# Kernel optimization log

Hardware: AMD Instinct MI355X
Metric: run time of the kernel (lower is better)

The kernel has to match this reference:

```python
import jax, jax.numpy as jnp
import numpy as np
import math

HIDDEN = 1024
HEADS = 16

def setup_inputs() -> dict:
    key = jax.random.key(0)
    k1, k2, k3 = jax.random.split(key, 3)
    B, T, C = 4, 2048, HIDDEN
    x = jax.random.normal(k1, (B, T, C), dtype=jnp.float32)
    w_qkv = jax.random.normal(k2, (C, 3 * C), dtype=jnp.float32) * (1.0 / math.sqrt(C))
    b_qkv = jnp.zeros((3 * C,), dtype=jnp.float32)
    w_out = jax.random.normal(k3, (C, C), dtype=jnp.float32) * (1.0 / math.sqrt(C))
    b_out = jnp.zeros((C,), dtype=jnp.float32)
    return {"x": x, "w_qkv": w_qkv, "b_qkv": b_qkv, "w_out": w_out, "b_out": b_out}

def reference(x, w_qkv, b_qkv, w_out, b_out):
    B, T, C = x.shape
    H = HEADS
    D = C // H  # head dim
    qkv = x @ w_qkv + b_qkv  # [B,T,3C]
    q, k, v = jnp.split(qkv, 3, axis=2)
    # [B,T,C] -> [B,H,T,D]
    q = q.reshape(B, T, H, D).transpose(0, 2, 1, 3)
    k = k.reshape(B, T, H, D).transpose(0, 2, 1, 3)
    v = v.reshape(B, T, H, D).transpose(0, 2, 1, 3)
    scale = 1.0 / math.sqrt(D)
    logits = jnp.einsum('bhqd,bhkd->bhqk', q, k) * scale  # [B,H,T,T]
    causal = jnp.tril(jnp.ones((T, T), dtype=bool))
    logits = jnp.where(causal[None, None, :, :], logits, -jnp.inf)
    probs = jax.nn.softmax(logits, axis=-1)
    out = jnp.einsum('bhqk,bhkd->bhqd', probs, v)  # [B,H,T,D]
    out = out.transpose(0, 2, 1, 3).reshape(B, T, C)
    return out @ w_out + b_out
```

## Files before the change

### kernel.cpp

```cpp
#include <hip/hip_runtime.h>
#include <hip/hip_bf16.h>

#define C_DIM  1024
#define NHEAD  16
#define DHEAD  64
#define T_LEN  2048
#define B_SZ   4
#define M_ROWS (B_SZ * T_LEN)
#define QKV_N  (3 * C_DIM)

typedef __bf16 bf16x8 __attribute__((ext_vector_type(8)));
typedef float  f32x4  __attribute__((ext_vector_type(4)));
typedef unsigned short ushort8_t __attribute__((ext_vector_type(8)));
typedef unsigned int   uint4_t   __attribute__((ext_vector_type(4)));

__device__ __forceinline__ unsigned short f2bf(float f) {
    union { float f; unsigned int u; } v; v.f = f;
    unsigned int r = v.u + 0x7FFFu + ((v.u >> 16) & 1u);
    return (unsigned short)(r >> 16);
}

__device__ __forceinline__ bf16x8 as_bf16x8(ushort8_t u) {
    return __builtin_bit_cast(bf16x8, u);
}

__device__ __forceinline__ f32x4 mfma16(bf16x8 a, bf16x8 b, f32x4 c) {
    return __builtin_amdgcn_mfma_f32_16x16x32_bf16(a, b, c, 0, 0, 0);
}

__device__ __forceinline__ void block_sync_lds() {
    asm volatile("s_waitcnt lgkmcnt(0)" ::: "memory");
    __builtin_amdgcn_s_barrier();
}

#define GLL16(gsrc, ldst) __builtin_amdgcn_global_load_lds( \
    (const __attribute__((address_space(1))) void*)(gsrc),  \
    (__attribute__((address_space(3))) void*)(ldst), 16, 0, 0)

__device__ __forceinline__ int xcd_remap(int id, int nwg) {
    const int q = nwg >> 3, r = nwg & 7;
    const int xcd = id & 7, off = id >> 3;
    return (xcd < r) ? (xcd * (q + 1) + off) : (r * (q + 1) + (xcd - r) * q + off);
}

__global__ void k_convert(const float* __restrict__ in, unsigned short* __restrict__ out, int n4) {
    int i = blockIdx.x * blockDim.x + threadIdx.x;
    if (i >= n4) return;
    const float4 v = ((const float4*)in)[i];
    unsigned int lo = (unsigned int)f2bf(v.x) | ((unsigned int)f2bf(v.y) << 16);
    unsigned int hi = (unsigned int)f2bf(v.z) | ((unsigned int)f2bf(v.w) << 16);
    ((uint2*)out)[i] = make_uint2(lo, hi);
}

__global__ void k_transpose_bf16(const float* __restrict__ w, unsigned short* __restrict__ wT,
                                 int K, int N) {
    __shared__ float tile[32][33];
    const int n0 = blockIdx.x * 32, k0 = blockIdx.y * 32;
    const int tx = threadIdx.x, ty = threadIdx.y;
    for (int i = 0; i < 32; i += 8)
        tile[ty + i][tx] = w[(size_t)(k0 + ty + i) * N + (n0 + tx)];
    __syncthreads();
    for (int i = 0; i < 32; i += 8)
        wT[(size_t)(n0 + ty + i) * K + (k0 + tx)] = f2bf(tile[tx][ty + i]);
}

__global__ void k_transpose_v(const unsigned short* __restrict__ qkv,
                              unsigned short* __restrict__ vtg) {
    __shared__ unsigned short tile[32][33];
    const int tt = blockIdx.x;
    const int dy = blockIdx.y;
    const int bh = dy >> 1, dtile = dy & 1;
    const int b = bh >> 4, h = bh & 15;
    const int t0 = tt * 32, d0 = dtile * 32;
    const int tx = threadIdx.x, ty = threadIdx.y;
    const unsigned short* src = qkv + (size_t)b * T_LEN * QKV_N + 2 * C_DIM + h * DHEAD + d0;
    for (int i = 0; i < 32; i += 8)
        tile[ty + i][tx] = src[(size_t)(t0 + ty + i) * QKV_N + tx];
    __syncthreads();
    unsigned short* dst = vtg + ((size_t)bh * DHEAD + d0) * T_LEN + t0;
    for (int i = 0; i < 32; i += 8)
        dst[(size_t)(ty + i) * T_LEN + tx] = tile[tx][ty + i];
}

template<int BF16_OUT>
__global__ __launch_bounds__(256) void k_gemm(const unsigned short* __restrict__ A,
                       const unsigned short* __restrict__ Bt,
                       const float* __restrict__ bias,
                       void* __restrict__ C,
                       unsigned short* __restrict__ vtg,
                       int M, int N, int K) {
    __shared__ unsigned short As[128][64];
    __shared__ unsigned short Bs[128][64];

    const int tid  = threadIdx.x;
    const int lane = tid & 63;
    const int wv   = tid >> 6;
    const int wm = wv >> 1, wn = wv & 1;

    const int nwg = gridDim.x * gridDim.y;
    const int wg  = xcd_remap(blockIdx.y * gridDim.x + blockIdx.x, nwg);
    const int bx = wg % gridDim.x, by = wg / gridDim.x;
    const int m0 = by * 128;
    const int n0 = bx * 128;
    const int lr = lane & 15, lg = lane >> 4;

    f32x4 acc[4][4];
#pragma unroll
    for (int i = 0; i < 4; i++)
#pragma unroll
        for (int j = 0; j < 4; j++) acc[i][j] = (f32x4){0.f, 0.f, 0.f, 0.f};

    const int gr = lane >> 3;
    const int gc = 8 * ((lane & 7) ^ gr);

    for (int kt = 0; kt < K; kt += 64) {
        __syncthreads();
#pragma unroll
        for (int j = 0; j < 4; j++) {
            const int row = 32 * wv + 8 * j;
            GLL16(A  + (size_t)(m0 + row + gr) * K + kt + gc, &As[row][0]);
            GLL16(Bt + (size_t)(n0 + row + gr) * K + kt + gc, &Bs[row][0]);
        }
        __syncthreads();

#pragma unroll
        for (int s = 0; s < 2; s++) {
            const int cb = (s * 64 + lg * 16) ^ ((lr & 7) << 4);
            bf16x8 af[4], bfr[4];
#pragma unroll
            for (int i = 0; i < 4; i++)
                af[i] = as_bf16x8(*(const ushort8_t*)((const char*)&As[wm * 64 + i * 16 + lr][0] + cb));
#pragma unroll
            for (int j = 0; j < 4; j++)
                bfr[j] = as_bf16x8(*(const ushort8_t*)((const char*)&Bs[wn * 64 + j * 16 + lr][0] + cb));
#pragma unroll
            for (int i = 0; i < 4; i++)
#pragma unroll
                for (int j = 0; j < 4; j++)
                    acc[i][j] = mfma16(af[i], bfr[j], acc[i][j]);
        }
    }

    const bool isV = (vtg != nullptr) && (n0 >= 2 * C_DIM);
#pragma unroll
    for (int i = 0; i < 4; i++) {
#pragma unroll
        for (int j = 0; j < 4; j++) {
            const int col = n0 + wn * 64 + j * 16 + lr;
            const float bv = bias ? bias[col] : 0.f;
            if (isV) {
                const int dcol = col - 2 * C_DIM;
                const int hh = dcol >> 6, dd = dcol & 63;
                const int row0 = m0 + wm * 64 + i * 16 + lg * 4;
                const int bb = row0 >> 11, t0 = row0 & (T_LEN - 1);
                const unsigned int p0 = (unsigned int)f2bf(acc[i][j][0] + bv)
                                      | ((unsigned int)f2bf(acc[i][j][1] + bv) << 16);
                const unsigned int p1 = (unsigned int)f2bf(acc[i][j][2] + bv)
                                      | ((unsigned int)f2bf(acc[i][j][3] + bv) << 16);
                *(uint2*)&vtg[(((size_t)(bb * 16 + hh)) * 64 + dd) * T_LEN + t0] = make_uint2(p0, p1);
            } else {
#pragma unroll
                for (int r = 0; r < 4; r++) {
                    const int row = m0 + wm * 64 + i * 16 + lg * 4 + r;
                    const float v = acc[i][j][r] + bv;
                    if (BF16_OUT)
                        ((unsigned short*)C)[(size_t)row * N + col] = f2bf(v);
                    else
                        ((float*)C)[(size_t)row * N + col] = v;
                }
            }
        }
    }
}

#define KS_OFF(B_, ROW_) (((B_) << 13) + ((ROW_) << 7))
#define VS_OFF(B_, ROW_) (16384 + ((B_) << 13) + ((ROW_) << 7))
#define SCALE2 0.180336880f
__global__ __launch_bounds__(256, 2) void k_attn(const unsigned short* __restrict__ qkv,
                                                 const unsigned short* __restrict__ vtg,
                                                 unsigned short* __restrict__ out) {
    __shared__ __align__(16) char smem[32768];

    const int blk = xcd_remap(blockIdx.x, B_SZ * NHEAD * 16);
    const int pr = blk & 15;
    const int h  = (blk >> 4) & 15;
    const int b  = blk >> 8;
    const int bh = b * 16 + h;

    const int tid  = threadIdx.x;
    const int lane = tid & 63;
    const int w    = tid >> 6;
    const int lr = lane & 15, lg = lane >> 4;
    const int gr = lane >> 3;
    const int gc = 8 * ((lane & 7) ^ gr);
    const int ra = w * 16;

    const int sA = lr + 32 * (lg & 1);
    const int sB = sA + 16;
    const int fhi = lg >> 1;

    const size_t base = (size_t)b * T_LEN * QKV_N + (size_t)h * DHEAD;
    const unsigned short* Qp = qkv + base;
    const unsigned short* Kp = qkv + base + C_DIM;
    const unsigned short* Vt = vtg + (size_t)bh * DHEAD * T_LEN;

    int buf = 0;
    for (int t = 0; t < 2; t++) {
        const int qt = (t == 0) ? pr : (31 - pr);
        const int qw = qt * 64 + w * 16;
        const int qg = qw + lr;
        const int R  = qt + 1;

        bf16x8 qf[2];
#pragma unroll
        for (int s = 0; s < 2; s++)
            qf[s] = as_bf16x8(*(const ushort8_t*)&Qp[(size_t)(qw + lr) * QKV_N + s * 32 + lg * 8]);

        f32x4 o[4];
#pragma unroll
        for (int f = 0; f < 4; f++) o[f] = (f32x4){0.f, 0.f, 0.f, 0.f};
        float lp = 0.f;

        GLL16(Kp + (size_t)(ra + gr) * QKV_N + gc,          smem + KS_OFF(buf, ra));
        GLL16(Kp + (size_t)(ra + 8 + gr) * QKV_N + gc,      smem + KS_OFF(buf, ra + 8));
        GLL16(Vt + (size_t)(ra + gr) * T_LEN + gc,          smem + VS_OFF(buf, ra));
        GLL16(Vt + (size_t)(ra + 8 + gr) * T_LEN + gc,      smem + VS_OFF(buf, ra + 8));

        for (int r = 0; r < R; ++r) {
            const int kb = r * 64;
            if (r + 1 < R) {
                const int kn = kb + 64;
                GLL16(Kp + (size_t)(kn + ra + gr) * QKV_N + gc,     smem + KS_OFF(buf ^ 1, ra));
                GLL16(Kp + (size_t)(kn + ra + 8 + gr) * QKV_N + gc, smem + KS_OFF(buf ^ 1, ra + 8));
                GLL16(Vt + (size_t)(ra + gr) * T_LEN + kn + gc,     smem + VS_OFF(buf ^ 1, ra));
                GLL16(Vt + (size_t)(ra + 8 + gr) * T_LEN + kn + gc, smem + VS_OFF(buf ^ 1, ra + 8));
                asm volatile("s_waitcnt vmcnt(4)" ::: "memory");
            } else {
                asm volatile("s_waitcnt vmcnt(0)" ::: "memory");
            }
            __builtin_amdgcn_s_barrier();
            __builtin_amdgcn_sched_barrier(0);

            f32x4 s4[4];
            __builtin_amdgcn_s_setprio(1);
#pragma unroll
            for (int f = 0; f < 4; f++) {
                const int row = f * 16 + lr;
                const bf16x8 kf0 = as_bf16x8(*(const ushort8_t*)
                    (smem + KS_OFF(buf, row) + ((lg * 16) ^ ((lr & 7) << 4))));
                const bf16x8 kf1 = as_bf16x8(*(const ushort8_t*)
                    (smem + KS_OFF(buf, row) + ((64 + lg * 16) ^ ((lr & 7) << 4))));
                f32x4 s = (f32x4){0.f, 0.f, 0.f, 0.f};
                s = mfma16(kf0, qf[0], s);
                s = mfma16(kf1, qf[1], s);
                s4[f] = s;
            }
            __builtin_amdgcn_s_setprio(0);

            const bool last = (r == R - 1);
            unsigned int Dk[4][2];
#pragma unroll
            for (int f = 0; f < 4; f++) {
                unsigned short hh[4];
#pragma unroll
                for (int rr = 0; rr < 4; rr++) {
                    float sv = fminf(s4[f][rr] * SCALE2, 72.f);
                    if (last) {
                        const int kg = kb + f * 16 + lg * 4 + rr;
                        if (kg > qg) sv = -1e30f;
                    }
                    const float e = __builtin_amdgcn_exp2f(sv);
                    lp += e;
                    hh[rr] = __builtin_bit_cast(unsigned short, (__bf16)e);
                }
                Dk[f][0] = (unsigned int)hh[0] | ((unsigned int)hh[1] << 16);
                Dk[f][1] = (unsigned int)hh[2] | ((unsigned int)hh[3] << 16);
            }

#pragma unroll
            for (int st = 0; st < 2; st++) {
                const int a0 = __shfl((int)Dk[2 * st][0],     sA, 64);
                const int b0 = __shfl((int)Dk[2 * st + 1][0], sA, 64);
                const int a1 = __shfl((int)Dk[2 * st][1],     sA, 64);
                const int b1 = __shfl((int)Dk[2 * st + 1][1], sA, 64);
                const int a2 = __shfl((int)Dk[2 * st][0],     sB, 64);
                const int b2 = __shfl((int)Dk[2 * st + 1][0], sB, 64);
                const int a3 = __shfl((int)Dk[2 * st][1],     sB, 64);
                const int b3 = __shfl((int)Dk[2 * st + 1][1], sB, 64);
                uint4_t pw;
                pw.x = (unsigned int)(fhi ? b0 : a0);
                pw.y = (unsigned int)(fhi ? b1 : a1);
                pw.z = (unsigned int)(fhi ? b2 : a2);
                pw.w = (unsigned int)(fhi ? b3 : a3);
                const bf16x8 pa = __builtin_bit_cast(bf16x8, pw);

                __builtin_amdgcn_s_setprio(1);
#pragma unroll
                for (int f = 0; f < 4; f++) {
                    const int row = f * 16 + lr;
                    const bf16x8 bv = as_bf16x8(*(const ushort8_t*)
                        (smem + VS_OFF(buf, row) + ((st * 64 + lg * 16) ^ ((lr & 7) << 4))));
                    o[f] = mfma16(pa, bv, o[f]);
                }
                __builtin_amdgcn_s_setprio(0);
            }

            block_sync_lds();
            buf ^= 1;
        }

        lp += __shfl_xor(lp, 16, 64);
        lp += __shfl_xor(lp, 32, 64);

        float inv[4];
#pragma unroll
        for (int rr = 0; rr < 4; rr++)
            inv[rr] = 1.f / __shfl(lp, lg * 4 + rr, 64);
#pragma unroll
        for (int rr = 0; rr < 4; rr++) {
            const int q = qw + lg * 4 + rr;
#pragma unroll
            for (int f = 0; f < 4; f++)
                out[((size_t)b * T_LEN + q) * C_DIM + h * DHEAD + f * 16 + lr] =
                    f2bf(o[f][rr] * inv[rr]);
        }
    }
}

extern "C" void kernel_launch(void* const* d_in, const int* in_sizes, int n_in,
                              void* d_out, int out_size, void* d_ws, size_t ws_size,
                              hipStream_t stream) {
    const float* x      = (const float*)d_in[0];
    const float* w_qkv  = (const float*)d_in[1];
    const float* b_qkv  = (const float*)d_in[2];
    const float* w_out  = (const float*)d_in[3];
    const float* b_out  = (const float*)d_in[4];
    float* out = (float*)d_out;

    char* ws = (char*)d_ws;
    unsigned short* xb    = (unsigned short*)(ws);
    unsigned short* wqkvT = (unsigned short*)(ws + 16777216);
    unsigned short* woutT = (unsigned short*)(ws + 16777216 + 6291456);
    unsigned short* qkv   = (unsigned short*)(ws + 25165824);
    unsigned short* attn  = (unsigned short*)(ws + 75497472);

    const size_t VTG_OFF = 92274688ull;
    const bool fused_vt = (ws_size >= VTG_OFF + 16777216ull);
    unsigned short* vtg = fused_vt ? (unsigned short*)(ws + VTG_OFF)
                                   : (unsigned short*)(ws);

    {
        const int n4 = M_ROWS * C_DIM / 4;
        k_convert<<<(n4 + 255) / 256, 256, 0, stream>>>(x, xb, n4);
    }
    k_transpose_bf16<<<dim3(QKV_N / 32, C_DIM / 32), dim3(32, 8), 0, stream>>>(w_qkv, wqkvT, C_DIM, QKV_N);
    k_transpose_bf16<<<dim3(C_DIM / 32, C_DIM / 32), dim3(32, 8), 0, stream>>>(w_out, woutT, C_DIM, C_DIM);
    k_gemm<1><<<dim3(QKV_N / 128, M_ROWS / 128), 256, 0, stream>>>(
        xb, wqkvT, b_qkv, qkv, fused_vt ? vtg : nullptr, M_ROWS, QKV_N, C_DIM);
    if (!fused_vt)
        k_transpose_v<<<dim3(T_LEN / 32, 64 * 2), dim3(32, 8), 0, stream>>>(qkv, vtg);
    k_attn<<<B_SZ * NHEAD * 16, 256, 0, stream>>>(qkv, vtg, attn);
    k_gemm<0><<<dim3(C_DIM / 128, M_ROWS / 128), 256, 0, stream>>>(
        attn, woutT, b_out, out, nullptr, M_ROWS, C_DIM, C_DIM);
}
```

Before: 173.5 us.

## Split attention keys across waves with per-wave K/V buffers and LDS reduction

Restructures the attention kernel so each wave handles all 64 query rows but only a 16-key slice of each 64-key block. Each wave loads and double-buffers its own K/V slice, which removes the per-iteration block barriers and the cross-lane shuffles for P. Partial outputs and row sums are reduced across the four waves through LDS at the end, and results are written as vectorized stores. Occupancy bounds are raised to 4 blocks. The PV MFMA now runs with half-zero K operands, which wastes MFMA throughput, and the final reduction adds extra LDS traffic and barriers.

```diff
diff --git a/kernel.cpp b/kernel.cpp
--- a/kernel.cpp
+++ b/kernel.cpp
@@ -26,11 +26,6 @@
 
 __device__ __forceinline__ f32x4 mfma16(bf16x8 a, bf16x8 b, f32x4 c) {
     return __builtin_amdgcn_mfma_f32_16x16x32_bf16(a, b, c, 0, 0, 0);
-}
-
-__device__ __forceinline__ void block_sync_lds() {
-    asm volatile("s_waitcnt lgkmcnt(0)" ::: "memory");
-    __builtin_amdgcn_s_barrier();
 }
 
 #define GLL16(gsrc, ldst) __builtin_amdgcn_global_load_lds( \
@@ -173,13 +168,16 @@
     }
 }
 
-#define KS_OFF(B_, ROW_) (((B_) << 13) + ((ROW_) << 7))
-#define VS_OFF(B_, ROW_) (16384 + ((B_) << 13) + ((ROW_) << 7))
+#define KS_OFF(W_, B_) ((W_) * 4096 + (B_) * 2048)
+#define VS_OFF(W_, B_) (16384 + (W_) * 4096 + (B_) * 2048)
+#define PART_OFF(W_)   ((W_) * 8704)
+#define LBUF_OFF       34816
 #define SCALE2 0.180336880f
-__global__ __launch_bounds__(256, 2) void k_attn(const unsigned short* __restrict__ qkv,
+__global__ __launch_bounds__(256, 4) void k_attn(const unsigned short* __restrict__ qkv,
                                                  const unsigned short* __restrict__ vtg,
                                                  unsigned short* __restrict__ out) {
-    __shared__ __align__(16) char smem[32768];
+    __shared__ __align__(16) char smem[35840];
+    float* smemf = (float*)smem;
 
     const int blk = xcd_remap(blockIdx.x, B_SZ * NHEAD * 16);
     const int pr = blk & 15;
@@ -191,13 +189,11 @@
     const int lane = tid & 63;
     const int w    = tid >> 6;
     const int lr = lane & 15, lg = lane >> 4;
+
     const int gr = lane >> 3;
     const int gc = 8 * ((lane & 7) ^ gr);
-    const int ra = w * 16;
-
-    const int sA = lr + 32 * (lg & 1);
-    const int sB = sA + 16;
-    const int fhi = lg >> 1;
+    const int vr = lane >> 1;
+    const int vc = 8 * ((lane & 1) ^ ((lane >> 3) & 1));
 
     const size_t base = (size_t)b * T_LEN * QKV_N + (size_t)h * DHEAD;
     const unsigned short* Qp = qkv + base;
@@ -207,122 +203,165 @@
     int buf = 0;
     for (int t = 0; t < 2; t++) {
         const int qt = (t == 0) ? pr : (31 - pr);
-        const int qw = qt * 64 + w * 16;
-        const int qg = qw + lr;
+        const int q0 = qt * 64;
         const int R  = qt + 1;
 
-        bf16x8 qf[2];
-#pragma unroll
-        for (int s = 0; s < 2; s++)
-            qf[s] = as_bf16x8(*(const ushort8_t*)&Qp[(size_t)(qw + lr) * QKV_N + s * 32 + lg * 8]);
-
-        f32x4 o[4];
-#pragma unroll
-        for (int f = 0; f < 4; f++) o[f] = (f32x4){0.f, 0.f, 0.f, 0.f};
-        float lp = 0.f;
-
-        GLL16(Kp + (size_t)(ra + gr) * QKV_N + gc,          smem + KS_OFF(buf, ra));
-        GLL16(Kp + (size_t)(ra + 8 + gr) * QKV_N + gc,      smem + KS_OFF(buf, ra + 8));
-        GLL16(Vt + (size_t)(ra + gr) * T_LEN + gc,          smem + VS_OFF(buf, ra));
-        GLL16(Vt + (size_t)(ra + 8 + gr) * T_LEN + gc,      smem + VS_OFF(buf, ra + 8));
+        bf16x8 qf[4][2];
+#pragma unroll
+        for (int fq = 0; fq < 4; fq++)
+#pragma unroll
+            for (int ks = 0; ks < 2; ks++)
+                qf[fq][ks] = as_bf16x8(*(const ushort8_t*)
+                    &Qp[(size_t)(q0 + fq * 16 + lr) * QKV_N + ks * 32 + lg * 8]);
+
+        f32x4 o[4][4];
+#pragma unroll
+        for (int fq = 0; fq < 4; fq++)
+#pragma unroll
+            for (int fd = 0; fd < 4; fd++) o[fq][fd] = (f32x4){0.f, 0.f, 0.f, 0.f};
+        float lp[4] = {0.f, 0.f, 0.f, 0.f};
+
+        {
+            const int kw = w * 16;
+            GLL16(Kp + (size_t)(kw + gr) * QKV_N + gc,         smem + KS_OFF(w, buf));
+            GLL16(Kp + (size_t)(kw + 8 + gr) * QKV_N + gc,     smem + KS_OFF(w, buf) + 1024);
+            GLL16(Vt + (size_t)vr * T_LEN + kw + vc,           smem + VS_OFF(w, buf));
+            GLL16(Vt + (size_t)(32 + vr) * T_LEN + kw + vc,    smem + VS_OFF(w, buf) + 1024);
+        }
 
         for (int r = 0; r < R; ++r) {
-            const int kb = r * 64;
+            const int kw = r * 64 + w * 16;
+
             if (r + 1 < R) {
-                const int kn = kb + 64;
-                GLL16(Kp + (size_t)(kn + ra + gr) * QKV_N + gc,     smem + KS_OFF(buf ^ 1, ra));
-                GLL16(Kp + (size_t)(kn + ra + 8 + gr) * QKV_N + gc, smem + KS_OFF(buf ^ 1, ra + 8));
-                GLL16(Vt + (size_t)(ra + gr) * T_LEN + kn + gc,     smem + VS_OFF(buf ^ 1, ra));
-                GLL16(Vt + (size_t)(ra + 8 + gr) * T_LEN + kn + gc, smem + VS_OFF(buf ^ 1, ra + 8));
+                const int kn = kw + 64;
+                GLL16(Kp + (size_t)(kn + gr) * QKV_N + gc,      smem + KS_OFF(w, buf ^ 1));
+                GLL16(Kp + (size_t)(kn + 8 + gr) * QKV_N + gc,  smem + KS_OFF(w, buf ^ 1) + 1024);
+                GLL16(Vt + (size_t)vr * T_LEN + kn + vc,        smem + VS_OFF(w, buf ^ 1));
+                GLL16(Vt + (size_t)(32 + vr) * T_LEN + kn + vc, smem + VS_OFF(w, buf ^ 1) + 1024);
                 asm volatile("s_waitcnt vmcnt(4)" ::: "memory");
             } else {
                 asm volatile("s_waitcnt vmcnt(0)" ::: "memory");
             }
-            __builtin_amdgcn_s_barrier();
             __builtin_amdgcn_sched_barrier(0);
+
+            uint2 vb[4];
+#pragma unroll
+            for (int fd = 0; fd < 4; fd++) {
+                const int d = fd * 16 + lr;
+                vb[fd] = *(const uint2*)(smem + VS_OFF(w, buf) +
+                         (d * 32 + ((lg * 8) ^ (((d >> 2) & 1) << 4))));
+            }
+
+            bf16x8 kf[2];
+#pragma unroll
+            for (int ks = 0; ks < 2; ks++)
+                kf[ks] = as_bf16x8(*(const ushort8_t*)(smem + KS_OFF(w, buf) +
+                          lr * 128 + ((ks * 64 + lg * 16) ^ ((lr & 7) << 4))));
 
             f32x4 s4[4];
             __builtin_amdgcn_s_setprio(1);
 #pragma unroll
-            for (int f = 0; f < 4; f++) {
-                const int row = f * 16 + lr;
-                const bf16x8 kf0 = as_bf16x8(*(const ushort8_t*)
-                    (smem + KS_OFF(buf, row) + ((lg * 16) ^ ((lr & 7) << 4))));
-                const bf16x8 kf1 = as_bf16x8(*(const ushort8_t*)
-                    (smem + KS_OFF(buf, row) + ((64 + lg * 16) ^ ((lr & 7) << 4))));
+            for (int fq = 0; fq < 4; fq++) {
                 f32x4 s = (f32x4){0.f, 0.f, 0.f, 0.f};
-                s = mfma16(kf0, qf[0], s);
-                s = mfma16(kf1, qf[1], s);
-                s4[f] = s;
+                s = mfma16(kf[0], qf[fq][0], s);
+                s = mfma16(kf[1], qf[fq][1], s);
+                s4[fq] = s;
             }
             __builtin_amdgcn_s_setprio(0);
 
             const bool last = (r == R - 1);
-            unsigned int Dk[4][2];
-#pragma unroll
-            for (int f = 0; f < 4; f++) {
+            bf16x8 pa[4];
+#pragma unroll
+            for (int fq = 0; fq < 4; fq++) {
                 unsigned short hh[4];
 #pragma unroll
                 for (int rr = 0; rr < 4; rr++) {
-                    float sv = fminf(s4[f][rr] * SCALE2, 72.f);
+                    float sv = fminf(s4[fq][rr] * SCALE2, 72.f);
                     if (last) {
-                        const int kg = kb + f * 16 + lg * 4 + rr;
+                        const int kg = kw + lg * 4 + rr;
+                        const int qg = q0 + fq * 16 + lr;
                         if (kg > qg) sv = -1e30f;
                     }
                     const float e = __builtin_amdgcn_exp2f(sv);
-                    lp += e;
+                    lp[fq] += e;
                     hh[rr] = __builtin_bit_cast(unsigned short, (__bf16)e);
                 }
-                Dk[f][0] = (unsigned int)hh[0] | ((unsigned int)hh[1] << 16);
-                Dk[f][1] = (unsigned int)hh[2] | ((unsigned int)hh[3] << 16);
-            }
-
-#pragma unroll
-            for (int st = 0; st < 2; st++) {
-                const int a0 = __shfl((int)Dk[2 * st][0],     sA, 64);
-                const int b0 = __shfl((int)Dk[2 * st + 1][0], sA, 64);
-                const int a1 = __shfl((int)Dk[2 * st][1],     sA, 64);
-                const int b1 = __shfl((int)Dk[2 * st + 1][1], sA, 64);
-                const int a2 = __shfl((int)Dk[2 * st][0],     sB, 64);
-                const int b2 = __shfl((int)Dk[2 * st + 1][0], sB, 64);
-                const int a3 = __shfl((int)Dk[2 * st][1],     sB, 64);
-                const int b3 = __shfl((int)Dk[2 * st + 1][1], sB, 64);
                 uint4_t pw;
-                pw.x = (unsigned int)(fhi ? b0 : a0);
-                pw.y = (unsigned int)(fhi ? b1 : a1);
-                pw.z = (unsigned int)(fhi ? b2 : a2);
-                pw.w = (unsigned int)(fhi ? b3 : a3);
-                const bf16x8 pa = __builtin_bit_cast(bf16x8, pw);
-
-                __builtin_amdgcn_s_setprio(1);
-#pragma unroll
-                for (int f = 0; f < 4; f++) {
-                    const int row = f * 16 + lr;
-                    const bf16x8 bv = as_bf16x8(*(const ushort8_t*)
-                        (smem + VS_OFF(buf, row) + ((st * 64 + lg * 16) ^ ((lr & 7) << 4))));
-                    o[f] = mfma16(pa, bv, o[f]);
+                pw.x = (unsigned int)hh[0] | ((unsigned int)hh[1] << 16);
+                pw.y = (unsigned int)hh[2] | ((unsigned int)hh[3] << 16);
+                pw.z = 0u;
+                pw.w = 0u;
+                pa[fq] = __builtin_bit_cast(bf16x8, pw);
+            }
+
+            __builtin_amdgcn_s_setprio(1);
+#pragma unroll
+            for (int fd = 0; fd < 4; fd++) {
+                uint4_t bw;
+                bw.x = vb[fd].x; bw.y = vb[fd].y;
+                bw.z = vb[fd].x; bw.w = vb[fd].y;
+                const bf16x8 bv = __builtin_bit_cast(bf16x8, bw);
+#pragma unroll
+                for (int fq = 0; fq < 4; fq++)
+                    o[fq][fd] = mfma16(pa[fq], bv, o[fq][fd]);
+            }
+            __builtin_amdgcn_s_setprio(0);
+            buf ^= 1;
+        }
+
+#pragma unroll
+        for (int fq = 0; fq < 4; fq++) {
+            lp[fq] += __shfl_xor(lp[fq], 16, 64);
+            lp[fq] += __shfl_xor(lp[fq], 32, 64);
+        }
+
+        __syncthreads();
+
+        if (lg == 0) {
+#pragma unroll
+            for (int fq = 0; fq < 4; fq++)
+                *(float*)(smem + LBUF_OFF + (w * 64 + fq * 16 + lr) * 4) = lp[fq];
+        }
+
+#pragma unroll
+        for (int half = 0; half < 2; half++) {
+#pragma unroll
+            for (int f2 = 0; f2 < 2; f2++) {
+                const int fq = half * 2 + f2;
+#pragma unroll
+                for (int fd = 0; fd < 4; fd++)
+#pragma unroll
+                    for (int rr = 0; rr < 4; rr++) {
+                        const int ql = f2 * 16 + lg * 4 + rr;
+                        smemf[(PART_OFF(w) >> 2) + ql * 68 + fd * 16 + lr] = o[fq][fd][rr];
+                    }
+            }
+            __syncthreads();
+
+            {
+                const int qrow = w * 8 + (lane >> 3);
+                const int d0 = (lane & 7) * 8;
+                f32x4 sA = (f32x4){0.f, 0.f, 0.f, 0.f};
+                f32x4 sB = (f32x4){0.f, 0.f, 0.f, 0.f};
+                float lt = 0.f;
+#pragma unroll
+                for (int pw = 0; pw < 4; pw++) {
+                    const int fbase = (PART_OFF(pw) >> 2) + qrow * 68 + d0;
+                    sA += *(const f32x4*)&smemf[fbase];
+                    sB += *(const f32x4*)&smemf[fbase + 4];
+                    lt += *(const float*)(smem + LBUF_OFF + (pw * 64 + half * 32 + qrow) * 4);
                 }
-                __builtin_amdgcn_s_setprio(0);
-            }
-
-            block_sync_lds();
-            buf ^= 1;
-        }
-
-        lp += __shfl_xor(lp, 16, 64);
-        lp += __shfl_xor(lp, 32, 64);
-
-        float inv[4];
-#pragma unroll
-        for (int rr = 0; rr < 4; rr++)
-            inv[rr] = 1.f / __shfl(lp, lg * 4 + rr, 64);
-#pragma unroll
-        for (int rr = 0; rr < 4; rr++) {
-            const int q = qw + lg * 4 + rr;
-#pragma unroll
-            for (int f = 0; f < 4; f++)
-                out[((size_t)b * T_LEN + q) * C_DIM + h * DHEAD + f * 16 + lr] =
-                    f2bf(o[f][rr] * inv[rr]);
+                const float inv = 1.f / lt;
+                ushort8_t ov;
+#pragma unroll
+                for (int j = 0; j < 4; j++) {
+                    ov[j]     = f2bf(sA[j] * inv);
+                    ov[4 + j] = f2bf(sB[j] * inv);
+                }
+                const int q = q0 + half * 32 + qrow;
+                *(ushort8_t*)&out[((size_t)b * T_LEN + q) * C_DIM + h * DHEAD + d0] = ov;
+            }
+            __syncthreads();
         }
     }
 }
```

Result: slower. 364.5 us (+110.0%).
